# Performance work log

Hardware: AMD Instinct MI355X
Metric: run time of the kernel (lower is better)

## Reference

```python
import jax, jax.numpy as jnp
import numpy as np

IN_FEATURES = 4096
OUT_FEATURES = 16384
B, S = 8, 16  # small token count -> weight-traffic bound (decode-like)


def setup_inputs() -> dict:
    key = jax.random.key(0)
    k_x, k_w, k_b = jax.random.split(key, 3)
    x = jax.random.normal(k_x, (B, S, IN_FEATURES), dtype=jnp.float32)
    # symmetric int8 quantized weight, values in [-127, 127]
    weight_int = jax.random.randint(k_w, (OUT_FEATURES, IN_FEATURES), -127, 128, dtype=jnp.int32)
    weight_scale = jnp.float32(0.01)      # scalar scale (symmetric, per-tensor)
    weight_zero_point = jnp.float32(0.0)  # symmetric -> zero_point = 0
    bias = jax.random.normal(k_b, (OUT_FEATURES,), dtype=jnp.float32)
    return {"x": x, "weight_int": weight_int, "weight_scale": weight_scale,
            "weight_zero_point": weight_zero_point, "bias": bias}


def reference(x, weight_int, weight_scale, weight_zero_point, bias):
    # dequantize: (q - zp) * scale, then F.linear: x @ W^T + b
    weight_float = (weight_int.astype(jnp.float32) - weight_zero_point) * weight_scale
    # x: [B, S, in], weight_float: [out, in] -> [B, S, out]
    return jnp.einsum('bsi,oi->bso', x, weight_float) + bias
```

## Files before the change

### kernel.cpp

```cpp
#include <hip/hip_runtime.h>
#include <hip/hip_bf16.h>


#define IN_F 4096
#define OUT_F 16384
#define NTOK 128

typedef __attribute__((ext_vector_type(8))) short bf16x8;
typedef __attribute__((ext_vector_type(4))) float f32x4;

__device__ __forceinline__ unsigned short f32_to_bf16_rne(float f) {
  unsigned u = __float_as_uint(f);
  u += 0x7fffu + ((u >> 16) & 1u);
  return (unsigned short)(u >> 16);
}

__global__ __launch_bounds__(512) void prep_x(const float* __restrict__ x,
                                              uint4* __restrict__ xf,
                                              float* __restrict__ xsum) {
  const int token = blockIdx.x;
  const int i = (int)threadIdx.x;
  const int k0 = i << 3;
  const float4 v0 = *(const float4*)(x + token * IN_F + k0);
  const float4 v1 = *(const float4*)(x + token * IN_F + k0 + 4);
  float v[8] = {v0.x, v0.y, v0.z, v0.w, v1.x, v1.y, v1.z, v1.w};
  unsigned short h[8];
  float s = 0.f;
#pragma unroll
  for (int j = 0; j < 8; ++j) {
    s += v[j];
    h[j] = f32_to_bf16_rne(v[j]);
  }
  uint4 o;
  o.x = (unsigned)h[0] | ((unsigned)h[1] << 16);
  o.y = (unsigned)h[2] | ((unsigned)h[3] << 16);
  o.z = (unsigned)h[4] | ((unsigned)h[5] << 16);
  o.w = (unsigned)h[6] | ((unsigned)h[7] << 16);
  const int slab = i >> 2;
  const int q = i & 3;
  const int lane = (q << 4) | (token & 15);
  xf[slab * 512 + (token >> 4) * 64 + lane] = o;

#pragma unroll
  for (int off = 32; off > 0; off >>= 1) s += __shfl_down(s, off, 64);
  __shared__ float wsum[8];
  if ((i & 63) == 0) wsum[i >> 6] = s;
  __syncthreads();
  if (i == 0) {
    float t = 0.f;
#pragma unroll
    for (int a = 0; a < 8; ++a) t += wsum[a];
    xsum[token] = t;
  }
}

__global__ __launch_bounds__(256, 1) void qlinear_main(
    const int* __restrict__ W, const uint4* __restrict__ xf,
    const float* __restrict__ xsum, const float* __restrict__ scale_p,
    const float* __restrict__ zp_p, const float* __restrict__ bias,
    float* __restrict__ out) {
  __shared__ float red[2 * 64 * 64];

  const int tid = (int)threadIdx.x;
  const int wave = tid >> 6;
  const int l = tid & 63;
  const int q = l >> 4;
  const int r = l & 15;
  const int rg = wave & 1;
  const int kh = wave >> 1;
  const int o_base = (int)blockIdx.x * 64 + rg * 32;

  const int* Wp0 = W + (o_base + r) * IN_F + kh * 2048 + q * 8;
  const int* Wp1 = W + (o_base + 16 + r) * IN_F + kh * 2048 + q * 8;
  const uint4* xp = xf + kh * 64 * 512 + l;

  f32x4 acc[2][8];
#pragma unroll
  for (int n = 0; n < 2; ++n)
#pragma unroll
    for (int t = 0; t < 8; ++t) acc[n][t] = (f32x4)0.0f;

  int4 a0A, a0B, a1A, a1B;
  int4 c0A, c0B, c1A, c1B;
  uint4 b0[8], b1[8];

  a0A = *(const int4*)(Wp0);
  a0B = *(const int4*)(Wp0 + 4);
  a1A = *(const int4*)(Wp1);
  a1B = *(const int4*)(Wp1 + 4);
#pragma unroll
  for (int t = 0; t < 8; ++t) b0[t] = xp[t * 64];

  for (int s = 0; s < 64; s += 2) {
    {
      const int sp = s + 1;
      c0A = *(const int4*)(Wp0 + sp * 32);
      c0B = *(const int4*)(Wp0 + sp * 32 + 4);
      c1A = *(const int4*)(Wp1 + sp * 32);
      c1B = *(const int4*)(Wp1 + sp * 32 + 4);
#pragma unroll
      for (int t = 0; t < 8; ++t) b1[t] = xp[sp * 512 + t * 64];
    }
    {
      bf16x8 af0, af1;
      af0[0] = (short)(__float_as_uint((float)a0A.x) >> 16);
      af0[1] = (short)(__float_as_uint((float)a0A.y) >> 16);
      af0[2] = (short)(__float_as_uint((float)a0A.z) >> 16);
      af0[3] = (short)(__float_as_uint((float)a0A.w) >> 16);
      af0[4] = (short)(__float_as_uint((float)a0B.x) >> 16);
      af0[5] = (short)(__float_as_uint((float)a0B.y) >> 16);
      af0[6] = (short)(__float_as_uint((float)a0B.z) >> 16);
      af0[7] = (short)(__float_as_uint((float)a0B.w) >> 16);
      af1[0] = (short)(__float_as_uint((float)a1A.x) >> 16);
      af1[1] = (short)(__float_as_uint((float)a1A.y) >> 16);
      af1[2] = (short)(__float_as_uint((float)a1A.z) >> 16);
      af1[3] = (short)(__float_as_uint((float)a1A.w) >> 16);
      af1[4] = (short)(__float_as_uint((float)a1B.x) >> 16);
      af1[5] = (short)(__float_as_uint((float)a1B.y) >> 16);
      af1[6] = (short)(__float_as_uint((float)a1B.z) >> 16);
      af1[7] = (short)(__float_as_uint((float)a1B.w) >> 16);
#pragma unroll
      for (int t = 0; t < 8; ++t) {
        bf16x8 bf = *(const bf16x8*)&b0[t];
        acc[0][t] = __builtin_amdgcn_mfma_f32_16x16x32_bf16(af0, bf, acc[0][t], 0, 0, 0);
        acc[1][t] = __builtin_amdgcn_mfma_f32_16x16x32_bf16(af1, bf, acc[1][t], 0, 0, 0);
      }
    }
    {
      const int sp = (s + 2 < 64) ? (s + 2) : 63;
      a0A = *(const int4*)(Wp0 + sp * 32);
      a0B = *(const int4*)(Wp0 + sp * 32 + 4);
      a1A = *(const int4*)(Wp1 + sp * 32);
      a1B = *(const int4*)(Wp1 + sp * 32 + 4);
#pragma unroll
      for (int t = 0; t < 8; ++t) b0[t] = xp[sp * 512 + t * 64];
    }
    {
      bf16x8 af0, af1;
      af0[0] = (short)(__float_as_uint((float)c0A.x) >> 16);
      af0[1] = (short)(__float_as_uint((float)c0A.y) >> 16);
      af0[2] = (short)(__float_as_uint((float)c0A.z) >> 16);
      af0[3] = (short)(__float_as_uint((float)c0A.w) >> 16);
      af0[4] = (short)(__float_as_uint((float)c0B.x) >> 16);
      af0[5] = (short)(__float_as_uint((float)c0B.y) >> 16);
      af0[6] = (short)(__float_as_uint((float)c0B.z) >> 16);
      af0[7] = (short)(__float_as_uint((float)c0B.w) >> 16);
      af1[0] = (short)(__float_as_uint((float)c1A.x) >> 16);
      af1[1] = (short)(__float_as_uint((float)c1A.y) >> 16);
      af1[2] = (short)(__float_as_uint((float)c1A.z) >> 16);
      af1[3] = (short)(__float_as_uint((float)c1A.w) >> 16);
      af1[4] = (short)(__float_as_uint((float)c1B.x) >> 16);
      af1[5] = (short)(__float_as_uint((float)c1B.y) >> 16);
      af1[6] = (short)(__float_as_uint((float)c1B.z) >> 16);
      af1[7] = (short)(__float_as_uint((float)c1B.w) >> 16);
#pragma unroll
      for (int t = 0; t < 8; ++t) {
        bf16x8 bf = *(const bf16x8*)&b1[t];
        acc[0][t] = __builtin_amdgcn_mfma_f32_16x16x32_bf16(af0, bf, acc[0][t], 0, 0, 0);
        acc[1][t] = __builtin_amdgcn_mfma_f32_16x16x32_bf16(af1, bf, acc[1][t], 0, 0, 0);
      }
    }
  }

  if (kh == 1) {
#pragma unroll
    for (int n = 0; n < 2; ++n)
#pragma unroll
      for (int t = 0; t < 8; ++t)
#pragma unroll
        for (int e = 0; e < 4; ++e)
          red[rg * 4096 + ((n * 8 + t) * 4 + e) * 64 + l] = acc[n][t][e];
  }
  __syncthreads();
  if (kh == 0) {
    const float scale = *scale_p;
    const float zp = *zp_p;
    const float czp = scale * zp;
    float4 bv0 = *(const float4*)(bias + o_base + q * 4);
    float4 bv1 = *(const float4*)(bias + o_base + 16 + q * 4);
#pragma unroll
    for (int t = 0; t < 8; ++t) {
      const int token = t * 16 + r;
      const float corr = -czp * xsum[token];
      float* orow = out + token * OUT_F + o_base + q * 4;
#pragma unroll
      for (int n = 0; n < 2; ++n) {
        const int base = rg * 4096 + ((n * 8 + t) * 4) * 64 + l;
        float4 o;
        o.x = (acc[n][t][0] + red[base + 0 * 64]) * scale + corr;
        o.y = (acc[n][t][1] + red[base + 1 * 64]) * scale + corr;
        o.z = (acc[n][t][2] + red[base + 2 * 64]) * scale + corr;
        o.w = (acc[n][t][3] + red[base + 3 * 64]) * scale + corr;
        if (n == 0) {
          o.x += bv0.x; o.y += bv0.y; o.z += bv0.z; o.w += bv0.w;
        } else {
          o.x += bv1.x; o.y += bv1.y; o.z += bv1.z; o.w += bv1.w;
        }
        *(float4*)(orow + n * 16) = o;
      }
    }
  }
}

extern "C" void kernel_launch(void* const* d_in, const int* in_sizes, int n_in,
                              void* d_out, int out_size, void* d_ws, size_t ws_size,
                              hipStream_t stream) {
  const float* x = (const float*)d_in[0];
  const int* W = (const int*)d_in[1];
  const float* scale = (const float*)d_in[2];
  const float* zp = (const float*)d_in[3];
  const float* bias = (const float*)d_in[4];
  float* out = (float*)d_out;

  uint4* xf = (uint4*)d_ws;
  float* xsum = (float*)((char*)d_ws + (1 << 20));

  prep_x<<<NTOK, 512, 0, stream>>>(x, xf, xsum);
  qlinear_main<<<OUT_F / 64, 256, 0, stream>>>(W, xf, xsum, scale, zp, bias, out);
}
```

Before: 419.2 us.

## Stage weight tiles through LDS with coalesced loads and 4-way K split

Each block now handles 32 output rows instead of 64, with four waves splitting K into quarters. Weight tiles are loaded in a row-coalesced pattern (8 rows by 32 ints per wave) and staged through per-wave double-buffered LDS before being converted to bf16 for MFMA. The starting K offset is staggered per block to spread DRAM channel access, and occupancy is raised to 2 blocks per CU. The final cross-wave reduction is spread across all waves. The costs are more LDS traffic and a larger shared reduction.

```diff
diff --git a/kernel.cpp b/kernel.cpp
--- a/kernel.cpp
+++ b/kernel.cpp
@@ -54,25 +54,42 @@
   }
 }
 
-__global__ __launch_bounds__(256, 1) void qlinear_main(
+__device__ __forceinline__ bf16x8 cvt8(int4 a, int4 b) {
+  bf16x8 o;
+  o[0] = (short)(__float_as_uint((float)a.x) >> 16);
+  o[1] = (short)(__float_as_uint((float)a.y) >> 16);
+  o[2] = (short)(__float_as_uint((float)a.z) >> 16);
+  o[3] = (short)(__float_as_uint((float)a.w) >> 16);
+  o[4] = (short)(__float_as_uint((float)b.x) >> 16);
+  o[5] = (short)(__float_as_uint((float)b.y) >> 16);
+  o[6] = (short)(__float_as_uint((float)b.z) >> 16);
+  o[7] = (short)(__float_as_uint((float)b.w) >> 16);
+  return o;
+}
+
+__global__ __launch_bounds__(256, 2) void qlinear_main(
     const int* __restrict__ W, const uint4* __restrict__ xf,
     const float* __restrict__ xsum, const float* __restrict__ scale_p,
     const float* __restrict__ zp_p, const float* __restrict__ bias,
     float* __restrict__ out) {
-  __shared__ float red[2 * 64 * 64];
+  __shared__ int smem[16384];
 
   const int tid = (int)threadIdx.x;
-  const int wave = tid >> 6;
+  const int w = tid >> 6;
   const int l = tid & 63;
   const int q = l >> 4;
   const int r = l & 15;
-  const int rg = wave & 1;
-  const int kh = wave >> 1;
-  const int o_base = (int)blockIdx.x * 64 + rg * 32;
-
-  const int* Wp0 = W + (o_base + r) * IN_F + kh * 2048 + q * 8;
-  const int* Wp1 = W + (o_base + 16 + r) * IN_F + kh * 2048 + q * 8;
-  const uint4* xp = xf + kh * 64 * 512 + l;
+  const int R0 = (int)blockIdx.x * 32;
+
+  const int row_l = l >> 3;
+  const int col_l = (l & 7) * 4;
+  const int* Wl = W + (R0 + row_l) * IN_F + w * 1024 + col_l;
+  const uint4* xp = xf + (w * 32) * 512 + l;
+
+  int* const sw = smem + w * 2048;
+  int* const sdl = sw + row_l * 32 + col_l;
+  const int* const srl0 = sw + r * 32 + q * 8;
+  const int* const srl1 = sw + (16 + r) * 32 + q * 8;
 
   f32x4 acc[2][8];
 #pragma unroll
@@ -80,125 +97,121 @@
 #pragma unroll
     for (int t = 0; t < 8; ++t) acc[n][t] = (f32x4)0.0f;
 
-  int4 a0A, a0B, a1A, a1B;
-  int4 c0A, c0B, c1A, c1B;
-  uint4 b0[8], b1[8];
-
-  a0A = *(const int4*)(Wp0);
-  a0B = *(const int4*)(Wp0 + 4);
-  a1A = *(const int4*)(Wp1);
-  a1B = *(const int4*)(Wp1 + 4);
-#pragma unroll
-  for (int t = 0; t < 8; ++t) b0[t] = xp[t * 64];
-
-  for (int s = 0; s < 64; s += 2) {
+  const int kk0 = ((int)blockIdx.x * 7) & 31;
+
+  uint4 B0[8], B1[8];
+  int4 G0, G1, G2, G3;
+
+  {
+    const int kk = kk0;
+    G0 = *(const int4*)(Wl + kk * 32);
+    G1 = *(const int4*)(Wl + 8 * IN_F + kk * 32);
+    G2 = *(const int4*)(Wl + 16 * IN_F + kk * 32);
+    G3 = *(const int4*)(Wl + 24 * IN_F + kk * 32);
+#pragma unroll
+    for (int t = 0; t < 8; ++t) B0[t] = xp[kk * 512 + t * 64];
+    *(int4*)(sdl + 0) = G0;
+    *(int4*)(sdl + 256) = G1;
+    *(int4*)(sdl + 512) = G2;
+    *(int4*)(sdl + 768) = G3;
+  }
+
+  for (int it = 0; it < 16; ++it) {
+    const int i2 = it * 2;
+    const int kkB = (kk0 + i2 + 1) & 31;
+    const int kkC = (kk0 + i2 + 2) & 31;
+
+    G0 = *(const int4*)(Wl + kkB * 32);
+    G1 = *(const int4*)(Wl + 8 * IN_F + kkB * 32);
+    G2 = *(const int4*)(Wl + 16 * IN_F + kkB * 32);
+    G3 = *(const int4*)(Wl + 24 * IN_F + kkB * 32);
+#pragma unroll
+    for (int t = 0; t < 8; ++t) B1[t] = xp[kkB * 512 + t * 64];
+
     {
-      const int sp = s + 1;
-      c0A = *(const int4*)(Wp0 + sp * 32);
-      c0B = *(const int4*)(Wp0 + sp * 32 + 4);
-      c1A = *(const int4*)(Wp1 + sp * 32);
-      c1B = *(const int4*)(Wp1 + sp * 32 + 4);
-#pragma unroll
-      for (int t = 0; t < 8; ++t) b1[t] = xp[sp * 512 + t * 64];
-    }
+      int4 x0 = *(const int4*)(srl0);
+      int4 x1 = *(const int4*)(srl0 + 4);
+      int4 y0 = *(const int4*)(srl1);
+      int4 y1 = *(const int4*)(srl1 + 4);
+      bf16x8 a0 = cvt8(x0, x1);
+      bf16x8 a1 = cvt8(y0, y1);
+#pragma unroll
+      for (int t = 0; t < 8; ++t) {
+        bf16x8 bf = *(const bf16x8*)&B0[t];
+        acc[0][t] = __builtin_amdgcn_mfma_f32_16x16x32_bf16(a0, bf, acc[0][t], 0, 0, 0);
+        acc[1][t] = __builtin_amdgcn_mfma_f32_16x16x32_bf16(a1, bf, acc[1][t], 0, 0, 0);
+      }
+    }
+    *(int4*)(sdl + 1024) = G0;
+    *(int4*)(sdl + 1024 + 256) = G1;
+    *(int4*)(sdl + 1024 + 512) = G2;
+    *(int4*)(sdl + 1024 + 768) = G3;
+
+    if (it != 15) {
+      G0 = *(const int4*)(Wl + kkC * 32);
+      G1 = *(const int4*)(Wl + 8 * IN_F + kkC * 32);
+      G2 = *(const int4*)(Wl + 16 * IN_F + kkC * 32);
+      G3 = *(const int4*)(Wl + 24 * IN_F + kkC * 32);
+#pragma unroll
+      for (int t = 0; t < 8; ++t) B0[t] = xp[kkC * 512 + t * 64];
+    }
+
     {
-      bf16x8 af0, af1;
-      af0[0] = (short)(__float_as_uint((float)a0A.x) >> 16);
-      af0[1] = (short)(__float_as_uint((float)a0A.y) >> 16);
-      af0[2] = (short)(__float_as_uint((float)a0A.z) >> 16);
-      af0[3] = (short)(__float_as_uint((float)a0A.w) >> 16);
-      af0[4] = (short)(__float_as_uint((float)a0B.x) >> 16);
-      af0[5] = (short)(__float_as_uint((float)a0B.y) >> 16);
-      af0[6] = (short)(__float_as_uint((float)a0B.z) >> 16);
-      af0[7] = (short)(__float_as_uint((float)a0B.w) >> 16);
-      af1[0] = (short)(__float_as_uint((float)a1A.x) >> 16);
-      af1[1] = (short)(__float_as_uint((float)a1A.y) >> 16);
-      af1[2] = (short)(__float_as_uint((float)a1A.z) >> 16);
-      af1[3] = (short)(__float_as_uint((float)a1A.w) >> 16);
-      af1[4] = (short)(__float_as_uint((float)a1B.x) >> 16);
-      af1[5] = (short)(__float_as_uint((float)a1B.y) >> 16);
-      af1[6] = (short)(__float_as_uint((float)a1B.z) >> 16);
-      af1[7] = (short)(__float_as_uint((float)a1B.w) >> 16);
+      int4 x0 = *(const int4*)(srl0 + 1024);
+      int4 x1 = *(const int4*)(srl0 + 1024 + 4);
+      int4 y0 = *(const int4*)(srl1 + 1024);
+      int4 y1 = *(const int4*)(srl1 + 1024 + 4);
+      bf16x8 a0 = cvt8(x0, x1);
+      bf16x8 a1 = cvt8(y0, y1);
 #pragma unroll
       for (int t = 0; t < 8; ++t) {
-        bf16x8 bf = *(const bf16x8*)&b0[t];
-        acc[0][t] = __builtin_amdgcn_mfma_f32_16x16x32_bf16(af0, bf, acc[0][t], 0, 0, 0);
-        acc[1][t] = __builtin_amdgcn_mfma_f32_16x16x32_bf16(af1, bf, acc[1][t], 0, 0, 0);
+        bf16x8 bf = *(const bf16x8*)&B1[t];
+        acc[0][t] = __builtin_amdgcn_mfma_f32_16x16x32_bf16(a0, bf, acc[0][t], 0, 0, 0);
+        acc[1][t] = __builtin_amdgcn_mfma_f32_16x16x32_bf16(a1, bf, acc[1][t], 0, 0, 0);
       }
     }
-    {
-      const int sp = (s + 2 < 64) ? (s + 2) : 63;
-      a0A = *(const int4*)(Wp0 + sp * 32);
-      a0B = *(const int4*)(Wp0 + sp * 32 + 4);
-      a1A = *(const int4*)(Wp1 + sp * 32);
-      a1B = *(const int4*)(Wp1 + sp * 32 + 4);
-#pragma unroll
-      for (int t = 0; t < 8; ++t) b0[t] = xp[sp * 512 + t * 64];
-    }
-    {
-      bf16x8 af0, af1;
-      af0[0] = (short)(__float_as_uint((float)c0A.x) >> 16);
-      af0[1] = (short)(__float_as_uint((float)c0A.y) >> 16);
-      af0[2] = (short)(__float_as_uint((float)c0A.z) >> 16);
-      af0[3] = (short)(__float_as_uint((float)c0A.w) >> 16);
-      af0[4] = (short)(__float_as_uint((float)c0B.x) >> 16);
-      af0[5] = (short)(__float_as_uint((float)c0B.y) >> 16);
-      af0[6] = (short)(__float_as_uint((float)c0B.z) >> 16);
-      af0[7] = (short)(__float_as_uint((float)c0B.w) >> 16);
-      af1[0] = (short)(__float_as_uint((float)c1A.x) >> 16);
-      af1[1] = (short)(__float_as_uint((float)c1A.y) >> 16);
-      af1[2] = (short)(__float_as_uint((float)c1A.z) >> 16);
-      af1[3] = (short)(__float_as_uint((float)c1A.w) >> 16);
-      af1[4] = (short)(__float_as_uint((float)c1B.x) >> 16);
-      af1[5] = (short)(__float_as_uint((float)c1B.y) >> 16);
-      af1[6] = (short)(__float_as_uint((float)c1B.z) >> 16);
-      af1[7] = (short)(__float_as_uint((float)c1B.w) >> 16);
-#pragma unroll
-      for (int t = 0; t < 8; ++t) {
-        bf16x8 bf = *(const bf16x8*)&b1[t];
-        acc[0][t] = __builtin_amdgcn_mfma_f32_16x16x32_bf16(af0, bf, acc[0][t], 0, 0, 0);
-        acc[1][t] = __builtin_amdgcn_mfma_f32_16x16x32_bf16(af1, bf, acc[1][t], 0, 0, 0);
-      }
-    }
-  }
-
-  if (kh == 1) {
+    if (it != 15) {
+      *(int4*)(sdl + 0) = G0;
+      *(int4*)(sdl + 256) = G1;
+      *(int4*)(sdl + 512) = G2;
+      *(int4*)(sdl + 768) = G3;
+    }
+  }
+
+  __syncthreads();
+  {
+    float* sp = (float*)smem;
 #pragma unroll
     for (int n = 0; n < 2; ++n)
 #pragma unroll
       for (int t = 0; t < 8; ++t)
-#pragma unroll
-        for (int e = 0; e < 4; ++e)
-          red[rg * 4096 + ((n * 8 + t) * 4 + e) * 64 + l] = acc[n][t][e];
+        *(f32x4*)(sp + w * 4096 + (n * 8 + t) * 256 + l * 4) = acc[n][t];
   }
   __syncthreads();
-  if (kh == 0) {
-    const float scale = *scale_p;
-    const float zp = *zp_p;
-    const float czp = scale * zp;
-    float4 bv0 = *(const float4*)(bias + o_base + q * 4);
-    float4 bv1 = *(const float4*)(bias + o_base + 16 + q * 4);
-#pragma unroll
-    for (int t = 0; t < 8; ++t) {
-      const int token = t * 16 + r;
-      const float corr = -czp * xsum[token];
-      float* orow = out + token * OUT_F + o_base + q * 4;
-#pragma unroll
-      for (int n = 0; n < 2; ++n) {
-        const int base = rg * 4096 + ((n * 8 + t) * 4) * 64 + l;
-        float4 o;
-        o.x = (acc[n][t][0] + red[base + 0 * 64]) * scale + corr;
-        o.y = (acc[n][t][1] + red[base + 1 * 64]) * scale + corr;
-        o.z = (acc[n][t][2] + red[base + 2 * 64]) * scale + corr;
-        o.w = (acc[n][t][3] + red[base + 3 * 64]) * scale + corr;
-        if (n == 0) {
-          o.x += bv0.x; o.y += bv0.y; o.z += bv0.z; o.w += bv0.w;
-        } else {
-          o.x += bv1.x; o.y += bv1.y; o.z += bv1.z; o.w += bv1.w;
-        }
-        *(float4*)(orow + n * 16) = o;
-      }
-    }
+  const float scale = *scale_p;
+  const float zp = *zp_p;
+  const float czp = scale * zp;
+  const float* sp = (const float*)smem;
+#pragma unroll
+  for (int j = 0; j < 4; ++j) {
+    const int c = w * 4 + j;
+    const int n = c >> 3;
+    const int t = c & 7;
+    f32x4 s0 = *(const f32x4*)(sp + 0 * 4096 + c * 256 + l * 4);
+    f32x4 s1 = *(const f32x4*)(sp + 1 * 4096 + c * 256 + l * 4);
+    f32x4 s2 = *(const f32x4*)(sp + 2 * 4096 + c * 256 + l * 4);
+    f32x4 s3 = *(const f32x4*)(sp + 3 * 4096 + c * 256 + l * 4);
+    f32x4 s = (s0 + s1) + (s2 + s3);
+    const int token = t * 16 + r;
+    const float corr = -czp * xsum[token];
+    const int feat = R0 + n * 16 + q * 4;
+    const float4 bv = *(const float4*)(bias + feat);
+    float4 o;
+    o.x = s[0] * scale + corr + bv.x;
+    o.y = s[1] * scale + corr + bv.y;
+    o.z = s[2] * scale + corr + bv.z;
+    o.w = s[3] * scale + corr + bv.w;
+    *(float4*)(out + token * OUT_F + feat) = o;
   }
 }
 
@@ -216,5 +229,5 @@
   float* xsum = (float*)((char*)d_ws + (1 << 20));
 
   prep_x<<<NTOK, 512, 0, stream>>>(x, xf, xsum);
-  qlinear_main<<<OUT_F / 64, 256, 0, stream>>>(W, xf, xsum, scale, zp, bias, out);
-}
+  qlinear_main<<<OUT_F / 32, 256, 0, stream>>>(W, xf, xsum, scale, zp, bias, out);
+}
```

After: 378.8 us. 1.11x faster.
